# Performance work log

Measured on AMD Instinct MI355X. Metric: run time of the kernel, lower is better.

Reference implementation:

```python
import jax, jax.numpy as jnp
import numpy as np

N, R, DIN, DOUT = 4096, 16, 256, 256


def setup_inputs() -> dict:
    key = jax.random.key(0)
    k1, k2, k3, k4 = jax.random.split(key, 4)
    x = jax.random.normal(k1, (N, DIN), dtype=jnp.float32)
    relations = jax.random.randint(k2, (N,), 0, R, dtype=jnp.int32)
    # kaiming-uniform-ish init for w, uniform bound for bias (as in reset_parameters)
    bound = 1.0 / np.sqrt(DIN).astype(np.float32)
    w = jax.random.uniform(k3, (R, DIN, DOUT), dtype=jnp.float32, minval=-bound, maxval=bound)
    bias = jax.random.uniform(k4, (R, DOUT), dtype=jnp.float32, minval=-bound, maxval=bound)
    return {"x": x, "relations": relations, "w": w, "bias": bias}


def reference(x, relations, w, bias):
    # out[n] = x[n] @ w[relations[n]] + bias[relations[n]]
    w_g = jnp.take(w, relations, axis=0)          # [N, DIN, DOUT] gathered per-row weights
    out = jnp.einsum('ni,nio->no', x, w_g)        # per-sample matmul
    out = out + jnp.take(bias, relations, axis=0)  # [N, DOUT]
    return out
```

## Files before the change

kernel.cpp:

```cpp
#include <hip/hip_runtime.h>
#include <hip/hip_bf16.h>

#define N_ROWS 4096
#define R_REL  16
#define DIN    256
#define DOUT   256
#define BM     32
#define GX     16

typedef __attribute__((ext_vector_type(4))) float f32x4;
typedef __attribute__((ext_vector_type(8))) short s16x8;
typedef unsigned long long u64;

__device__ __forceinline__ short f2bf(float f) {
    union { float f; unsigned u; } v; v.f = f;
    unsigned r = v.u + 0x7FFFu + ((v.u >> 16) & 1u);
    return (short)(r >> 16);
}

__global__ __launch_bounds__(256) void prep_kernel(
        const float* __restrict__ w, const int* __restrict__ rel,
        ushort* __restrict__ wF, int* __restrict__ perm, int* __restrict__ cnt) {
    const int b = blockIdx.x, t = threadIdx.x;
    if (b < 128) {
        const int r = b >> 3, ks = b & 7;
        const float* src = w + ((size_t)r * DIN + ks * 32) * DOUT + t;
        ushort* dst = wF + (((size_t)r * 8 + ks) * 256 + t) * 32;
        s16x8 o[4];
        #pragma unroll
        for (int q = 0; q < 4; ++q)
            #pragma unroll
            for (int j = 0; j < 8; ++j)
                o[q][j] = f2bf(src[(size_t)(q * 8 + j) * DOUT]);
        #pragma unroll
        for (int q = 0; q < 4; ++q)
            *(s16x8*)(dst + q * 8) = o[q];
    } else {
        const int r = b - 128;
        __shared__ int cur;
        if (t == 0) cur = 0;
        __syncthreads();
        const int lane = t & 63;
        const u64 ltmask = (1ull << lane) - 1ull;
        int* permr = perm + r * N_ROWS;
        #pragma unroll
        for (int it = 0; it < 16; ++it) {
            const int n = it * 256 + t;
            const bool match = (rel[n] == r);
            const u64 m = __ballot(match);
            int wbase = 0;
            if (lane == 0 && m) wbase = atomicAdd(&cur, (int)__popcll(m));
            wbase = __shfl(wbase, 0);
            if (match) permr[wbase + (int)__popcll(m & ltmask)] = n;
        }
        __syncthreads();
        if (t == 0) cnt[r] = cur;
    }
}

__global__ __launch_bounds__(256) void rgemm_kernel(
        const float* __restrict__ x, const ushort* __restrict__ wF,
        const float* __restrict__ bias, const int* __restrict__ cnt,
        const int* __restrict__ perm, float* __restrict__ out) {
    const int r     = blockIdx.y;
    const int ch    = blockIdx.z;
    const int count = cnt[r];
    const int t     = threadIdx.x;
    const int lane  = t & 63, wv = t >> 6;
    const int frow  = lane & 15, kgrp = lane >> 4;

    __shared__ int    rowidx[BM];
    __shared__ ushort A[BM][264];

    const int col0 = ch * 128 + wv * 32;
    const float bv0 = bias[r * DOUT + col0 + frow];
    const float bv1 = bias[r * DOUT + col0 + 16 + frow];
    const int*    permr = perm + r * N_ROWS;
    const ushort* wFr   = wF + (size_t)r * 8 * 256 * 32;

    for (int tile = blockIdx.x; tile * BM < count; tile += GX) {
        const int row0 = tile * BM;
        __syncthreads();
        if (t < BM) {
            const int idx = row0 + t;
            rowidx[t] = permr[idx < count ? idx : count - 1];
        }
        __syncthreads();
        {
            const int rl = t >> 3, seg = t & 7;
            const float* src = x + (size_t)rowidx[rl] * DIN + seg * 32;
            #pragma unroll
            for (int q = 0; q < 4; ++q) {
                const f32x4 v0 = *(const f32x4*)(src + q * 8);
                const f32x4 v1 = *(const f32x4*)(src + q * 8 + 4);
                s16x8 o;
                o[0]=f2bf(v0[0]); o[1]=f2bf(v0[1]); o[2]=f2bf(v0[2]); o[3]=f2bf(v0[3]);
                o[4]=f2bf(v1[0]); o[5]=f2bf(v1[1]); o[6]=f2bf(v1[2]); o[7]=f2bf(v1[3]);
                *(s16x8*)&A[rl][seg * 32 + q * 8] = o;
            }
        }
        __syncthreads();

        f32x4 acc[2][2] = {};
        #pragma unroll
        for (int ks = 0; ks < 8; ++ks) {
            const ushort* wb = wFr + (((size_t)ks * 256) + col0 + frow) * 32 + kgrp * 8;
            const s16x8 bf0 = *(const s16x8*)wb;
            const s16x8 bf1 = *(const s16x8*)(wb + 16 * 32);
            const s16x8 af0 = *(const s16x8*)&A[frow][ks * 32 + kgrp * 8];
            const s16x8 af1 = *(const s16x8*)&A[16 + frow][ks * 32 + kgrp * 8];
            acc[0][0] = __builtin_amdgcn_mfma_f32_16x16x32_bf16(af0, bf0, acc[0][0], 0, 0, 0);
            acc[1][0] = __builtin_amdgcn_mfma_f32_16x16x32_bf16(af1, bf0, acc[1][0], 0, 0, 0);
            acc[0][1] = __builtin_amdgcn_mfma_f32_16x16x32_bf16(af0, bf1, acc[0][1], 0, 0, 0);
            acc[1][1] = __builtin_amdgcn_mfma_f32_16x16x32_bf16(af1, bf1, acc[1][1], 0, 0, 0);
        }

        #pragma unroll
        for (int n = 0; n < 2; ++n) {
            const int col = col0 + n * 16 + frow;
            const float bv = n ? bv1 : bv0;
            #pragma unroll
            for (int m = 0; m < 2; ++m) {
                #pragma unroll
                for (int v = 0; v < 4; ++v) {
                    const int rl = m * 16 + kgrp * 4 + v;
                    if (row0 + rl < count)
                        out[(size_t)rowidx[rl] * DOUT + col] = acc[m][n][v] + bv;
                }
            }
        }
    }
}

extern "C" void kernel_launch(void* const* d_in, const int* in_sizes, int n_in,
                              void* d_out, int out_size, void* d_ws, size_t ws_size,
                              hipStream_t stream) {
    const float* x    = (const float*)d_in[0];
    const int*   rel  = (const int*)  d_in[1];
    const float* w    = (const float*)d_in[2];
    const float* bias = (const float*)d_in[3];
    float*       out  = (float*)d_out;

    char* ws = (char*)d_ws;
    int*    cnt  = (int*)ws;
    int*    perm = (int*)(ws + 0x100);
    ushort* wF   = (ushort*)(ws + 0x50000);

    prep_kernel<<<144, 256, 0, stream>>>(w, rel, wF, perm, cnt);

    dim3 grid(GX, R_REL, 2);
    rgemm_kernel<<<grid, 256, 0, stream>>>(x, wF, bias, cnt, perm, out);
}
```

Baseline: 20.67 us.

## Fuse relation bucketing and weight conversion into single grouped GEMM kernel

Removes the separate prep kernel. Each block now recomputes the per-relation row ranks with ballots and a shuffle-based prefix scan, and converts its fp32 weight slice to bf16 on the fly into a double-buffered shared-memory stage. The aim is to cut one kernel launch and the global round trip of the permuted indices and converted weights. In exchange, every tile redoes the ballot scan over the cached relation values and the weight conversion is repeated per tile, with a barrier added per k-step.

```diff
diff --git a/kernel.cpp b/kernel.cpp
--- a/kernel.cpp
+++ b/kernel.cpp
@@ -1,12 +1,11 @@
 #include <hip/hip_runtime.h>
-#include <hip/hip_bf16.h>
 
-#define N_ROWS 4096
-#define R_REL  16
-#define DIN    256
-#define DOUT   256
-#define BM     32
-#define GX     16
+#define R_REL 16
+#define DIN   256
+#define DOUT  256
+#define BM    32
+#define GX    16
+#define CHUNK 128
 
 typedef __attribute__((ext_vector_type(4))) float f32x4;
 typedef __attribute__((ext_vector_type(8))) short s16x8;
@@ -18,74 +17,75 @@
     return (short)(r >> 16);
 }
 
-__global__ __launch_bounds__(256) void prep_kernel(
-        const float* __restrict__ w, const int* __restrict__ rel,
-        ushort* __restrict__ wF, int* __restrict__ perm, int* __restrict__ cnt) {
-    const int b = blockIdx.x, t = threadIdx.x;
-    if (b < 128) {
-        const int r = b >> 3, ks = b & 7;
-        const float* src = w + ((size_t)r * DIN + ks * 32) * DOUT + t;
-        ushort* dst = wF + (((size_t)r * 8 + ks) * 256 + t) * 32;
-        s16x8 o[4];
-        #pragma unroll
-        for (int q = 0; q < 4; ++q)
-            #pragma unroll
-            for (int j = 0; j < 8; ++j)
-                o[q][j] = f2bf(src[(size_t)(q * 8 + j) * DOUT]);
-        #pragma unroll
-        for (int q = 0; q < 4; ++q)
-            *(s16x8*)(dst + q * 8) = o[q];
-    } else {
-        const int r = b - 128;
-        __shared__ int cur;
-        if (t == 0) cur = 0;
-        __syncthreads();
-        const int lane = t & 63;
-        const u64 ltmask = (1ull << lane) - 1ull;
-        int* permr = perm + r * N_ROWS;
-        #pragma unroll
-        for (int it = 0; it < 16; ++it) {
-            const int n = it * 256 + t;
-            const bool match = (rel[n] == r);
-            const u64 m = __ballot(match);
-            int wbase = 0;
-            if (lane == 0 && m) wbase = atomicAdd(&cur, (int)__popcll(m));
-            wbase = __shfl(wbase, 0);
-            if (match) permr[wbase + (int)__popcll(m & ltmask)] = n;
-        }
-        __syncthreads();
-        if (t == 0) cnt[r] = cur;
-    }
-}
+#define MFMA(a, b, c) __builtin_amdgcn_mfma_f32_16x16x32_bf16(a, b, c, 0, 0, 0)
 
-__global__ __launch_bounds__(256) void rgemm_kernel(
-        const float* __restrict__ x, const ushort* __restrict__ wF,
-        const float* __restrict__ bias, const int* __restrict__ cnt,
-        const int* __restrict__ perm, float* __restrict__ out) {
-    const int r     = blockIdx.y;
-    const int ch    = blockIdx.z;
-    const int count = cnt[r];
-    const int t     = threadIdx.x;
-    const int lane  = t & 63, wv = t >> 6;
-    const int frow  = lane & 15, kgrp = lane >> 4;
+__global__ __launch_bounds__(256) void fused_kernel(
+        const float* __restrict__ x, const int* __restrict__ rel,
+        const float* __restrict__ w, const float* __restrict__ bias,
+        float* __restrict__ out) {
+    const int r    = blockIdx.y;
+    const int ch   = blockIdx.z;
+    const int t    = threadIdx.x;
+    const int lane = t & 63, wv = t >> 6;
+    const int frow = lane & 15, kgrp = lane >> 4;
 
+    __shared__ int    wcnt[65];
     __shared__ int    rowidx[BM];
     __shared__ ushort A[BM][264];
+    __shared__ ushort Bc[2][CHUNK][40];
 
-    const int col0 = ch * 128 + wv * 32;
-    const float bv0 = bias[r * DOUT + col0 + frow];
-    const float bv1 = bias[r * DOUT + col0 + 16 + frow];
-    const int*    permr = perm + r * N_ROWS;
-    const ushort* wFr   = wF + (size_t)r * 8 * 256 * 32;
+    int myrel[16];
+    #pragma unroll
+    for (int it = 0; it < 16; ++it)
+        myrel[it] = rel[wv * 1024 + it * 64 + lane];
+
+    #pragma unroll
+    for (int it = 0; it < 16; ++it) {
+        const u64 m = __ballot(myrel[it] == r);
+        if (lane == 0) wcnt[wv * 16 + it] = (int)__popcll(m);
+    }
+    __syncthreads();
+    if (wv == 0) {
+        int c = wcnt[lane];
+        const int orig = c;
+        #pragma unroll
+        for (int d = 1; d < 64; d <<= 1) {
+            const int u = __shfl_up(c, d);
+            if (lane >= d) c += u;
+        }
+        wcnt[lane] = c - orig;
+        if (lane == 63) wcnt[64] = c;
+    }
+    __syncthreads();
+    const int count = wcnt[64];
+
+    const int col0 = ch * CHUNK;
+    const int colw = col0 + wv * 32;
+    const float bv0 = bias[r * DOUT + colw + frow];
+    const float bv1 = bias[r * DOUT + colw + 16 + frow];
+
+    const u64 ltmask = (1ull << lane) - 1ull;
+    const int half  = t >> 7;
+    const int colr  = t & 127;
+    const float* wcol = w + (size_t)r * DIN * DOUT + col0 + colr;
 
     for (int tile = blockIdx.x; tile * BM < count; tile += GX) {
         const int row0 = tile * BM;
         __syncthreads();
-        if (t < BM) {
-            const int idx = row0 + t;
-            rowidx[t] = permr[idx < count ? idx : count - 1];
+
+        if (t < BM && row0 + t >= count) rowidx[t] = 0;
+        #pragma unroll
+        for (int it = 0; it < 16; ++it) {
+            const bool match = (myrel[it] == r);
+            const u64 m = __ballot(match);
+            if (match) {
+                const int rank = wcnt[wv * 16 + it] + (int)__popcll(m & ltmask);
+                const int s = rank - row0;
+                if (s >= 0 && s < BM) rowidx[s] = wv * 1024 + it * 64 + lane;
+            }
         }
         __syncthreads();
+
         {
             const int rl = t >> 3, seg = t & 7;
             const float* src = x + (size_t)rowidx[rl] * DIN + seg * 32;
@@ -99,25 +99,49 @@
                 *(s16x8*)&A[rl][seg * 32 + q * 8] = o;
             }
         }
-        __syncthreads();
+
+        float g[16];
+        #pragma unroll
+        for (int i = 0; i < 16; ++i)
+            g[i] = wcol[(size_t)(half * 16 + i) * DOUT];
 
         f32x4 acc[2][2] = {};
         #pragma unroll
         for (int ks = 0; ks < 8; ++ks) {
-            const ushort* wb = wFr + (((size_t)ks * 256) + col0 + frow) * 32 + kgrp * 8;
-            const s16x8 bf0 = *(const s16x8*)wb;
-            const s16x8 bf1 = *(const s16x8*)(wb + 16 * 32);
+            s16x8 o0, o1;
+            #pragma unroll
+            for (int i = 0; i < 8; ++i) { o0[i] = f2bf(g[i]); o1[i] = f2bf(g[8 + i]); }
+            {
+                ushort* dst = &Bc[ks & 1][colr][half * 16];
+                *(s16x8*)dst       = o0;
+                *(s16x8*)(dst + 8) = o1;
+            }
+            float gn[16];
+            if (ks < 7) {
+                #pragma unroll
+                for (int i = 0; i < 16; ++i)
+                    gn[i] = wcol[(size_t)((ks + 1) * 32 + half * 16 + i) * DOUT];
+            }
+            __syncthreads();
+
             const s16x8 af0 = *(const s16x8*)&A[frow][ks * 32 + kgrp * 8];
             const s16x8 af1 = *(const s16x8*)&A[16 + frow][ks * 32 + kgrp * 8];
-            acc[0][0] = __builtin_amdgcn_mfma_f32_16x16x32_bf16(af0, bf0, acc[0][0], 0, 0, 0);
-            acc[1][0] = __builtin_amdgcn_mfma_f32_16x16x32_bf16(af1, bf0, acc[1][0], 0, 0, 0);
-            acc[0][1] = __builtin_amdgcn_mfma_f32_16x16x32_bf16(af0, bf1, acc[0][1], 0, 0, 0);
-            acc[1][1] = __builtin_amdgcn_mfma_f32_16x16x32_bf16(af1, bf1, acc[1][1], 0, 0, 0);
+            const s16x8 bf0 = *(const s16x8*)&Bc[ks & 1][wv * 32 + frow][kgrp * 8];
+            const s16x8 bf1 = *(const s16x8*)&Bc[ks & 1][wv * 32 + 16 + frow][kgrp * 8];
+            acc[0][0] = MFMA(af0, bf0, acc[0][0]);
+            acc[1][0] = MFMA(af1, bf0, acc[1][0]);
+            acc[0][1] = MFMA(af0, bf1, acc[0][1]);
+            acc[1][1] = MFMA(af1, bf1, acc[1][1]);
+
+            if (ks < 7) {
+                #pragma unroll
+                for (int i = 0; i < 16; ++i) g[i] = gn[i];
+            }
         }
 
         #pragma unroll
         for (int n = 0; n < 2; ++n) {
-            const int col = col0 + n * 16 + frow;
+            const int col = colw + n * 16 + frow;
             const float bv = n ? bv1 : bv0;
             #pragma unroll
             for (int m = 0; m < 2; ++m) {
@@ -141,13 +165,6 @@
     const float* bias = (const float*)d_in[3];
     float*       out  = (float*)d_out;
 
-    char* ws = (char*)d_ws;
-    int*    cnt  = (int*)ws;
-    int*    perm = (int*)(ws + 0x100);
-    ushort* wF   = (ushort*)(ws + 0x50000);
-
-    prep_kernel<<<144, 256, 0, stream>>>(w, rel, wF, perm, cnt);
-
     dim3 grid(GX, R_REL, 2);
-    rgemm_kernel<<<grid, 256, 0, stream>>>(x, wF, bias, cnt, perm, out);
+    fused_kernel<<<grid, 256, 0, stream>>>(x, rel, w, bias, out);
 }
```

New measurement: 17.93 us. 1.15x faster.
